# Optimization experiments

Measured on AMD Instinct MI355X. Metric: run time of the kernel, lower is better.

## Reference

```python
import jax, jax.numpy as jnp
import numpy as np

BLOCK_SIZE = 32
# NVFP4 decode table: index bit3 = sign, bits0-2 = magnitude code
DECODE = jnp.array([0.0, 0.5, 1.0, 1.5, 2.0, 3.0, 4.0, 6.0,
                    -0.0, -0.5, -1.0, -1.5, -2.0, -3.0, -4.0, -6.0], dtype=jnp.float32)

N_OUT, K_IN = 16384, 4096


def setup_inputs() -> dict:
    key = jax.random.key(0)
    k1, k2, k3, k4 = jax.random.split(key, 4)
    x = jax.random.normal(k1, (4, 512, K_IN), dtype=jnp.float32)
    # packed uint8 stored as int32 in [0, 256)
    weight_packed = jax.random.randint(k2, (N_OUT, K_IN // 2), 0, 256, dtype=jnp.int32)
    # per-block positive scales (block_max / 6.0 in the original)
    weight_scales = jax.random.uniform(k3, (N_OUT, K_IN // BLOCK_SIZE), dtype=jnp.float32,
                                       minval=1e-3, maxval=5e-2)
    bias = jax.random.normal(k4, (N_OUT,), dtype=jnp.float32) * 0.02
    return {"x": x, "weight_packed": weight_packed, "weight_scales": weight_scales, "bias": bias}


def _dequant(weight_packed, weight_scales):
    # unpack: low nibble -> even K index, high nibble -> odd K index
    low = DECODE[weight_packed & 15]           # [N, K//2]
    high = DECODE[(weight_packed >> 4) & 15]   # [N, K//2]
    n = weight_packed.shape[0]
    w = jnp.stack([low, high], axis=-1).reshape(n, -1)  # [N, K], interleaved
    # expand per-block scales along K
    scales = jnp.repeat(weight_scales, BLOCK_SIZE, axis=1)  # [N, K]
    return w * scales


def reference(x, weight_packed, weight_scales, bias):
    w = _dequant(weight_packed, weight_scales)            # [N, K]
    out = jnp.einsum('bsk,nk->bsn', x, w) + bias          # [B, S, N]
    # activation='gelu' -> F.gelu(approximate='tanh')
    return jax.nn.gelu(out, approximate=True)
```

## Files before the change

### kernel.cpp

```cpp
#include <hip/hip_runtime.h>
#include <hip/hip_bf16.h>

typedef short bf16x8 __attribute__((ext_vector_type(8)));
typedef float f32x4 __attribute__((ext_vector_type(4)));

#define K_DIM 4096
#define N_DIM 16384
#define M_DIM 2048
#define STRIPE 16384
#define TSTRIDE (64 * STRIPE)
#define WSB_BYTES ((size_t)N_DIM * K_DIM * 2)
#define WSA_BYTES ((size_t)M_DIM * K_DIM * 2)

__device__ __forceinline__ unsigned f2bf(float f) {
    unsigned u = __builtin_bit_cast(unsigned, f);
    u += 0x7FFFu + ((u >> 16) & 1u);
    return u >> 16;
}

__device__ __forceinline__ float dec4(unsigned c, float s) {
    unsigned mag = c & 7u;
    unsigned u = (mag >= 2u) ? ((((mag >> 1) + 126u) << 23) | ((mag & 1u) << 22))
                             : (mag == 1u ? 0x3F000000u : 0u);
    u |= (c & 8u) << 28;
    return __builtin_bit_cast(float, u) * s;
}

__device__ __forceinline__ float fexp2(float x) {
    float r; asm("v_exp_f32 %0, %1" : "=v"(r) : "v"(x)); return r;
}
__device__ __forceinline__ float gelu_tanh(float v) {
    float c = v + 0.044715f * v * v * v;
    float x = fminf(-2.3022084f * c, 80.0f);
    float t = fexp2(x);
    float th = (1.0f - t) * __builtin_amdgcn_rcpf(1.0f + t);
    return 0.5f * v * (1.0f + th);
}

__global__ __launch_bounds__(256) void dequant_w(const int* __restrict__ wp,
                                                 const float* __restrict__ wsc,
                                                 unsigned char* __restrict__ dst) {
    int t = blockIdx.x * 256 + threadIdx.x;
    int n = t >> 9;
    int ck = t & 511;
    int kstep = ck >> 3, s = ck & 7;
    int nt = n >> 7, r = n & 127;

    const int4 p4 = *reinterpret_cast<const int4*>(wp + (size_t)n * (K_DIM / 2) + kstep * 32 + s * 4);
    float scale = wsc[(size_t)n * (K_DIM / 32) + kstep * 2 + (s >> 2)];

    const int pv[4] = {p4.x, p4.y, p4.z, p4.w};
    unsigned o[8];
    #pragma unroll
    for (int j = 0; j < 4; ++j) {
        unsigned b = (unsigned)pv[j] & 255u;
        o[2 * j]     = f2bf(dec4(b & 15u, scale));
        o[2 * j + 1] = f2bf(dec4((b >> 4) & 15u, scale));
    }
    uint4 v;
    v.x = o[0] | (o[1] << 16);
    v.y = o[2] | (o[3] << 16);
    v.z = o[4] | (o[5] << 16);
    v.w = o[6] | (o[7] << 16);

    size_t off = (size_t)(nt * 64 + kstep) * STRIPE
               + (size_t)r * 128 + (size_t)((s ^ (r & 7)) << 4);
    *reinterpret_cast<uint4*>(dst + off) = v;
}

__global__ __launch_bounds__(256) void conv_x(const float* __restrict__ x,
                                              unsigned char* __restrict__ dst) {
    int t = blockIdx.x * 256 + threadIdx.x;
    int m = t >> 9;
    int ck = t & 511;
    int kstep = ck >> 3, s = ck & 7;
    int mt = m >> 7, r = m & 127;

    const float4* xp = reinterpret_cast<const float4*>(x + (size_t)m * K_DIM + kstep * 64 + s * 8);
    float4 a = xp[0], b = xp[1];
    uint4 v;
    v.x = f2bf(a.x) | (f2bf(a.y) << 16);
    v.y = f2bf(a.z) | (f2bf(a.w) << 16);
    v.z = f2bf(b.x) | (f2bf(b.y) << 16);
    v.w = f2bf(b.z) | (f2bf(b.w) << 16);

    size_t off = (size_t)(mt * 64 + kstep) * STRIPE
               + (size_t)r * 128 + (size_t)((s ^ (r & 7)) << 4);
    *reinterpret_cast<uint4*>(dst + off) = v;
}


__global__ __launch_bounds__(512, 2) void gemm_bf16_256(
    const unsigned char* __restrict__ wsA,
    const unsigned char* __restrict__ wsB,
    const float* __restrict__ bias,
    float* __restrict__ out)
{
    __shared__ unsigned char lds[131072];

    int id = blockIdx.x;
    int wg = (id & 7) * 64 + (id >> 3);
    int MT = wg & 7;
    int NT = wg >> 3;

    const int tid  = threadIdx.x;
    const int lane = tid & 63;
    const int w    = tid >> 6;
    const int wm   = w >> 2;
    const int wn   = w & 3;
    const int fr   = lane & 15;
    const int fg   = lane >> 4;

    const unsigned char* gA = wsA + (size_t)(2 * MT) * TSTRIDE;
    const unsigned char* gB = wsB + (size_t)(2 * NT) * TSTRIDE;

    int addrA[8];
    #pragma unroll
    for (int mi = 0; mi < 8; ++mi) {
        int row = wm * 128 + mi * 16 + fr;
        int L = row >> 1;
        addrA[mi] = L * 128 + (((((row & 1) << 2) | fg) ^ (L & 7)) << 4);
    }
    int addrB[4];
    #pragma unroll
    for (int ni = 0; ni < 4; ++ni) {
        int row = wn * 64 + ni * 16 + fr;
        int L = row >> 1;
        addrB[ni] = L * 128 + (((((row & 1) << 2) | fg) ^ (L & 7)) << 4);
    }

    int offST[2][2];
    #pragma unroll
    for (int j = 0; j < 2; ++j) {
        int c = w * 2 + j;
        int L = c * 8 + (lane >> 3);
        int p = lane & 7;
        int sl = p ^ (L & 7);
        int h = sl >> 2, fgs = sl & 3;
        int row = 2 * L + h;
        #pragma unroll
        for (int kb = 0; kb < 2; ++kb)
            offST[j][kb] = (row >> 7) * TSTRIDE + (row & 127) * 128
                         + ((((kb << 2) | fgs) ^ (row & 7)) << 4);
    }

#define GLDS(SRC, DOFF) __builtin_amdgcn_global_load_lds(                          \
        (const __attribute__((address_space(1))) unsigned int*)(SRC),              \
        (__attribute__((address_space(3))) unsigned int*)(&lds[DOFF]), 16, 0, 0)

#define STAGE_A(KSOFF, KB, SLOT) do {                                              \
        GLDS(gA + (KSOFF) + offST[0][KB], ((SLOT) << 14) + (w * 2 + 0) * 1024);    \
        GLDS(gA + (KSOFF) + offST[1][KB], ((SLOT) << 14) + (w * 2 + 1) * 1024);    \
    } while (0)
#define STAGE_B(KSOFF, KB, SLOT) do {                                              \
        GLDS(gB + (KSOFF) + offST[0][KB], 65536 + ((SLOT) << 14) + (w * 2 + 0) * 1024); \
        GLDS(gB + (KSOFF) + offST[1][KB], 65536 + ((SLOT) << 14) + (w * 2 + 1) * 1024); \
    } while (0)

#define READ_PF(PA, PB, SLOT) do {                                                 \
        const unsigned char* La_ = lds + ((SLOT) << 14);                           \
        const unsigned char* Lb_ = lds + 65536 + ((SLOT) << 14);                   \
        _Pragma("unroll") for (int ni = 0; ni < 4; ++ni)                           \
            PB[ni] = *reinterpret_cast<const bf16x8*>(Lb_ + addrB[ni]);            \
        _Pragma("unroll") for (int mi = 0; mi < 4; ++mi)                           \
            PA[mi] = *reinterpret_cast<const bf16x8*>(La_ + addrA[mi]);            \
    } while (0)

#define READ_KA(SLOT) do {                                                         \
        const unsigned char* Lk_ = lds + ((SLOT) << 14);                           \
        _Pragma("unroll") for (int mi = 0; mi < 4; ++mi)                           \
            ka[mi] = *reinterpret_cast<const bf16x8*>(Lk_ + addrA[4 + mi]);        \
    } while (0)

    f32x4 acc[8][4];
    #pragma unroll
    for (int mi = 0; mi < 8; ++mi)
        #pragma unroll
        for (int ni = 0; ni < 4; ++ni)
            acc[mi][ni] = (f32x4){0.f, 0.f, 0.f, 0.f};

    bf16x8 pa0[4], pb0[4], pa1[4], pb1[4];
    bf16x8 ka[4];

    STAGE_A(0, 0, 0);        STAGE_B(0, 0, 0);
    STAGE_A(0, 1, 1);        STAGE_B(0, 1, 1);
    STAGE_A(STRIPE, 0, 2);   STAGE_B(STRIPE, 0, 2);
    asm volatile("s_waitcnt vmcnt(4)" ::: "memory");
    __builtin_amdgcn_sched_barrier(0);
    __builtin_amdgcn_s_barrier();
    __builtin_amdgcn_sched_barrier(0);
    READ_PF(pa0, pb0, 0);
    READ_KA(0);

#define TILE_BODY(RSLOT, NSLOT, PA, PB, NPA, NPB, DO_STG, STKS, STKB, SSLOT, DO_PF, VMN) do { \
        if (DO_STG) STAGE_A(STKS, STKB, SSLOT);                                    \
        __builtin_amdgcn_s_setprio(1);                                             \
        _Pragma("unroll") for (int mi = 0; mi < 4; ++mi)                           \
            _Pragma("unroll") for (int ni = 0; ni < 4; ++ni)                       \
                acc[mi][ni] = __builtin_amdgcn_mfma_f32_16x16x32_bf16(             \
                    PA[mi], PB[ni], acc[mi][ni], 0, 0, 0);                         \
        __builtin_amdgcn_s_setprio(0);                                             \
        if (DO_STG) STAGE_B(STKS, STKB, SSLOT);                                    \
        if (DO_PF) READ_PF(NPA, NPB, NSLOT);                                       \
        __builtin_amdgcn_s_setprio(1);                                             \
        _Pragma("unroll") for (int mi = 0; mi < 4; ++mi)                           \
            _Pragma("unroll") for (int ni = 0; ni < 4; ++ni)                       \
                acc[4 + mi][ni] = __builtin_amdgcn_mfma_f32_16x16x32_bf16(         \
                    ka[mi], PB[ni], acc[4 + mi][ni], 0, 0, 0);                     \
        __builtin_amdgcn_s_setprio(0);                                             \
        if (DO_PF) READ_KA(NSLOT);                                                 \
        if ((VMN) >= 0) {                                                          \
            if ((VMN) == 4)      asm volatile("s_waitcnt vmcnt(4)" ::: "memory");  \
            else                 asm volatile("s_waitcnt vmcnt(0)" ::: "memory");  \
            __builtin_amdgcn_sched_barrier(0);                                     \
            __builtin_amdgcn_s_barrier();                                          \
            __builtin_amdgcn_sched_barrier(0);                                     \
        }                                                                          \
    } while (0)

    for (int tp = 0; tp < 62; ++tp) {
        const int scur = (tp & 1) << 1;
        const int ks1 = (tp + 1) * STRIPE;
        const int ks2 = (tp + 2) * STRIPE;
        TILE_BODY(scur,     scur ^ 1, pa0, pb0, pa1, pb1, 1, ks1, 1, scur ^ 3, 1, 4);
        TILE_BODY(scur ^ 1, scur ^ 2, pa1, pb1, pa0, pb0, 1, ks2, 0, scur,     1, 4);
    }
    TILE_BODY(0, 1, pa0, pb0, pa1, pb1, 1, 63 * STRIPE, 1, 3, 1, 4);
    TILE_BODY(1, 2, pa1, pb1, pa0, pb0, 0, 0, 0, 0, 1, 0);
    TILE_BODY(2, 3, pa0, pb0, pa1, pb1, 0, 0, 0, 0, 1, 0);
    TILE_BODY(3, 0, pa1, pb1, pa0, pb0, 0, 0, 0, 0, 0, -1);

    const int bm0 = MT * 256, bn0 = NT * 256;
    #pragma unroll
    for (int mi = 0; mi < 8; ++mi) {
        int row = bm0 + wm * 128 + mi * 16 + fg * 4;
        #pragma unroll
        for (int ni = 0; ni < 4; ++ni) {
            int col = bn0 + wn * 64 + ni * 16 + fr;
            float bv = bias[col];
            float* op = out + (size_t)row * N_DIM + col;
            #pragma unroll
            for (int q = 0; q < 4; ++q) {
                float v = acc[mi][ni][q] + bv;
                op[(size_t)q * N_DIM] = gelu_tanh(v);
            }
        }
    }
#undef TILE_BODY
#undef READ_KA
#undef READ_PF
#undef STAGE_A
#undef STAGE_B
#undef GLDS
}

__global__ __launch_bounds__(256, 2) void nvfp4_gemm(
    const float* __restrict__ x,
    const int*   __restrict__ wp,
    const float* __restrict__ wscale,
    const float* __restrict__ bias,
    float* __restrict__ out)
{
    __shared__ uint4  lsA[128 * 8];
    __shared__ uint4  lsB[128 * 8];
    __shared__ float2 lut[256];

    const int tid = threadIdx.x;
    {
        static const float dectab[16] = {0.f, 0.5f, 1.f, 1.5f, 2.f, 3.f, 4.f, 6.f,
                                         -0.f,-0.5f,-1.f,-1.5f,-2.f,-3.f,-4.f,-6.f};
        lut[tid] = make_float2(dectab[tid & 15], dectab[(tid >> 4) & 15]);
    }

    const int bn0 = blockIdx.x * 128;
    const int bm0 = blockIdx.y * 128;
    const int r = tid >> 1;
    const int h = tid & 1;

    const float4* xp = reinterpret_cast<const float4*>(x + (size_t)(bm0 + r) * K_DIM) + h * 8;
    const uint4*  bp = reinterpret_cast<const uint4*>(wp + (size_t)(bn0 + r) * (K_DIM / 2)) + h * 4;
    const float*  sp = wscale + (size_t)(bn0 + r) * (K_DIM / 32) + h;

    float4 ax[8];
    uint4  bx[4];
    float  scale;
    #pragma unroll
    for (int j = 0; j < 8; ++j) ax[j] = xp[j];
    #pragma unroll
    for (int q = 0; q < 4; ++q) bx[q] = bp[q];
    scale = sp[0];

    f32x4 acc[4][4];
    #pragma unroll
    for (int mi = 0; mi < 4; ++mi)
        #pragma unroll
        for (int ni = 0; ni < 4; ++ni)
            acc[mi][ni] = (f32x4){0.f, 0.f, 0.f, 0.f};

    const int lane = tid & 63;
    const int wid  = tid >> 6;
    const int wm0  = (wid >> 1) * 64;
    const int wn0  = (wid & 1) * 64;
    const int fr   = lane & 15;
    const int fg   = lane >> 4;

    __syncthreads();

    for (int kt = 0; kt < 64; ++kt) {
        #pragma unroll
        for (int j = 0; j < 4; ++j) {
            float4 f0 = ax[2 * j], f1 = ax[2 * j + 1];
            uint4 v;
            v.x = f2bf(f0.x) | (f2bf(f0.y) << 16);
            v.y = f2bf(f0.z) | (f2bf(f0.w) << 16);
            v.z = f2bf(f1.x) | (f2bf(f1.y) << 16);
            v.w = f2bf(f1.z) | (f2bf(f1.w) << 16);
            lsA[(r * 8 + h * 4 + j) ^ (r & 7)] = v;
        }
        #pragma unroll
        for (int q = 0; q < 4; ++q) {
            uint4 p = bx[q];
            float2 d0 = lut[p.x & 255];
            float2 d1 = lut[p.y & 255];
            float2 d2 = lut[p.z & 255];
            float2 d3 = lut[p.w & 255];
            uint4 v;
            v.x = f2bf(d0.x * scale) | (f2bf(d0.y * scale) << 16);
            v.y = f2bf(d1.x * scale) | (f2bf(d1.y * scale) << 16);
            v.z = f2bf(d2.x * scale) | (f2bf(d2.y * scale) << 16);
            v.w = f2bf(d3.x * scale) | (f2bf(d3.y * scale) << 16);
            lsB[(r * 8 + h * 4 + q) ^ (r & 7)] = v;
        }
        __syncthreads();

        if (kt + 1 < 64) {
            #pragma unroll
            for (int j = 0; j < 8; ++j) ax[j] = xp[(kt + 1) * 16 + j];
            #pragma unroll
            for (int q = 0; q < 4; ++q) bx[q] = bp[(kt + 1) * 8 + q];
            scale = sp[(kt + 1) * 2];
        }

        #pragma unroll
        for (int kk = 0; kk < 2; ++kk) {
            bf16x8 af[4], bfr[4];
            #pragma unroll
            for (int mi = 0; mi < 4; ++mi) {
                int row = wm0 + mi * 16 + fr;
                af[mi] = __builtin_bit_cast(bf16x8, lsA[(row * 8 + kk * 4 + fg) ^ (row & 7)]);
            }
            #pragma unroll
            for (int ni = 0; ni < 4; ++ni) {
                int row = wn0 + ni * 16 + fr;
                bfr[ni] = __builtin_bit_cast(bf16x8, lsB[(row * 8 + kk * 4 + fg) ^ (row & 7)]);
            }
            #pragma unroll
            for (int mi = 0; mi < 4; ++mi)
                #pragma unroll
                for (int ni = 0; ni < 4; ++ni)
                    acc[mi][ni] = __builtin_amdgcn_mfma_f32_16x16x32_bf16(
                        af[mi], bfr[ni], acc[mi][ni], 0, 0, 0);
        }
        __syncthreads();
    }

    #pragma unroll
    for (int mi = 0; mi < 4; ++mi) {
        int row = bm0 + wm0 + mi * 16 + fg * 4;
        #pragma unroll
        for (int ni = 0; ni < 4; ++ni) {
            int col = bn0 + wn0 + ni * 16 + fr;
            float bv = bias[col];
            float* op = out + (size_t)row * N_DIM + col;
            #pragma unroll
            for (int q = 0; q < 4; ++q) {
                float v = acc[mi][ni][q] + bv;
                op[(size_t)q * N_DIM] = gelu_tanh(v);
            }
        }
    }
}

extern "C" void kernel_launch(void* const* d_in, const int* in_sizes, int n_in,
                              void* d_out, int out_size, void* d_ws, size_t ws_size,
                              hipStream_t stream) {
    const float* x    = (const float*)d_in[0];
    const int*   wp   = (const int*)d_in[1];
    const float* wsc  = (const float*)d_in[2];
    const float* bias = (const float*)d_in[3];
    float*       out  = (float*)d_out;
    (void)in_sizes; (void)n_in; (void)out_size;

    if (ws_size >= WSB_BYTES + WSA_BYTES) {
        unsigned char* wsB = (unsigned char*)d_ws;
        unsigned char* wsA = wsB + WSB_BYTES;
        dequant_w<<<(N_DIM * (K_DIM / 8)) / 256, 256, 0, stream>>>(wp, wsc, wsB);
        conv_x<<<(M_DIM * (K_DIM / 8)) / 256, 256, 0, stream>>>(x, wsA);
        gemm_bf16_256<<<(M_DIM / 256) * (N_DIM / 256), 512, 0, stream>>>(wsA, wsB, bias, out);
    } else {
        dim3 grid(N_DIM / 128, M_DIM / 128);
        nvfp4_gemm<<<grid, 256, 0, stream>>>(x, wp, wsc, bias, out);
    }
}
```

Baseline: 296.8 us.

## Fuse dequant and activation conversion into GEMM with ticketed producer workgroups

Merges the weight dequant and x-to-bf16 conversion kernels into the GEMM launch. The first workgroup to claim each 256-row A or B panel via atomicCAS converts it into the workspace, publishes a done flag, and every workgroup spin-waits on the flags for its two panels before running the GEMM. The aim is to remove two kernel launches and overlap conversion with compute. The cost is a memset of the flags, spin-wait stalls, and a deadlock risk if producers are not resident. The intermediate-size workspace branch now falls back to the slow kernel, which looks unintended.

```diff
diff --git a/kernel.cpp b/kernel.cpp
--- a/kernel.cpp
+++ b/kernel.cpp
@@ -11,6 +11,7 @@
 #define TSTRIDE (64 * STRIPE)
 #define WSB_BYTES ((size_t)N_DIM * K_DIM * 2)
 #define WSA_BYTES ((size_t)M_DIM * K_DIM * 2)
+#define NUNITS 72
 
 __device__ __forceinline__ unsigned f2bf(float f) {
     unsigned u = __builtin_bit_cast(unsigned, f);
@@ -90,13 +91,18 @@
 }
 
 
-__global__ __launch_bounds__(512, 2) void gemm_bf16_256(
-    const unsigned char* __restrict__ wsA,
-    const unsigned char* __restrict__ wsB,
+__global__ __launch_bounds__(512, 2) void gemm_fused(
+    const int*   __restrict__ wp,
+    const float* __restrict__ wsc,
+    const float* __restrict__ x,
+    unsigned char* wsA,
+    unsigned char* wsB,
+    int* flags,
     const float* __restrict__ bias,
     float* __restrict__ out)
 {
     __shared__ unsigned char lds[131072];
+    __shared__ int s_role[2];
 
     int id = blockIdx.x;
     int wg = (id & 7) * 64 + (id >> 3);
@@ -110,6 +116,78 @@
     const int wn   = w & 3;
     const int fr   = lane & 15;
     const int fg   = lane >> 4;
+
+    int* tickets = flags;
+    int* done    = flags + NUNITS;
+    const int uA = MT;
+    const int uB = 8 + NT;
+
+    if (tid == 0) {
+        s_role[0] = (atomicCAS(&tickets[uA], 0, 1) == 0);
+        s_role[1] = (atomicCAS(&tickets[uB], 0, 1) == 0);
+    }
+    __syncthreads();
+
+    if (s_role[0]) {
+        for (int it = 0; it < 256; ++it) {
+            int g = it * 512 + tid;
+            int m = MT * 256 + (g >> 9);
+            int ck = g & 511;
+            int kstep = ck >> 3, s = ck & 7;
+            int mt = m >> 7, r = m & 127;
+            const float4* xp = reinterpret_cast<const float4*>(x + (size_t)m * K_DIM + kstep * 64 + s * 8);
+            float4 a = xp[0], b = xp[1];
+            uint4 v;
+            v.x = f2bf(a.x) | (f2bf(a.y) << 16);
+            v.y = f2bf(a.z) | (f2bf(a.w) << 16);
+            v.z = f2bf(b.x) | (f2bf(b.y) << 16);
+            v.w = f2bf(b.z) | (f2bf(b.w) << 16);
+            size_t off = (size_t)(mt * 64 + kstep) * STRIPE
+                       + (size_t)r * 128 + (size_t)((s ^ (r & 7)) << 4);
+            *reinterpret_cast<uint4*>(wsA + off) = v;
+        }
+    }
+    if (s_role[1]) {
+        for (int it = 0; it < 256; ++it) {
+            int g = it * 512 + tid;
+            int n = NT * 256 + (g >> 9);
+            int ck = g & 511;
+            int kstep = ck >> 3, s = ck & 7;
+            int nt = n >> 7, r = n & 127;
+            const int4 p4 = *reinterpret_cast<const int4*>(wp + (size_t)n * (K_DIM / 2) + kstep * 32 + s * 4);
+            float scale = wsc[(size_t)n * (K_DIM / 32) + kstep * 2 + (s >> 2)];
+            const int pv[4] = {p4.x, p4.y, p4.z, p4.w};
+            unsigned o[8];
+            #pragma unroll
+            for (int j = 0; j < 4; ++j) {
+                unsigned b = (unsigned)pv[j] & 255u;
+                o[2 * j]     = f2bf(dec4(b & 15u, scale));
+                o[2 * j + 1] = f2bf(dec4((b >> 4) & 15u, scale));
+            }
+            uint4 v;
+            v.x = o[0] | (o[1] << 16);
+            v.y = o[2] | (o[3] << 16);
+            v.z = o[4] | (o[5] << 16);
+            v.w = o[6] | (o[7] << 16);
+            size_t off = (size_t)(nt * 64 + kstep) * STRIPE
+                       + (size_t)r * 128 + (size_t)((s ^ (r & 7)) << 4);
+            *reinterpret_cast<uint4*>(wsB + off) = v;
+        }
+    }
+    if (s_role[0] || s_role[1]) {
+        __syncthreads();
+        if (tid == 0) {
+            __threadfence();
+            if (s_role[0]) atomicExch(&done[uA], 1);
+            if (s_role[1]) atomicExch(&done[uB], 1);
+        }
+    }
+    if (tid == 0) {
+        while (atomicAdd(&done[uA], 0) == 0) __builtin_amdgcn_s_sleep(8);
+        while (atomicAdd(&done[uB], 0) == 0) __builtin_amdgcn_s_sleep(8);
+    }
+    __syncthreads();
+    __threadfence();
 
     const unsigned char* gA = wsA + (size_t)(2 * MT) * TSTRIDE;
     const unsigned char* gB = wsB + (size_t)(2 * NT) * TSTRIDE;
@@ -391,12 +469,20 @@
     float*       out  = (float*)d_out;
     (void)in_sizes; (void)n_in; (void)out_size;
 
-    if (ws_size >= WSB_BYTES + WSA_BYTES) {
+    if (ws_size >= WSB_BYTES + WSA_BYTES + 1024) {
+        unsigned char* wsB = (unsigned char*)d_ws;
+        unsigned char* wsA = wsB + WSB_BYTES;
+        int* flags = (int*)(wsA + WSA_BYTES);
+        hipMemsetAsync(flags, 0, 1024, stream);
+        gemm_fused<<<(M_DIM / 256) * (N_DIM / 256), 512, 0, stream>>>(
+            wp, wsc, x, wsA, wsB, flags, bias, out);
+    } else if (ws_size >= WSB_BYTES + WSA_BYTES) {
         unsigned char* wsB = (unsigned char*)d_ws;
         unsigned char* wsA = wsB + WSB_BYTES;
         dequant_w<<<(N_DIM * (K_DIM / 8)) / 256, 256, 0, stream>>>(wp, wsc, wsB);
         conv_x<<<(M_DIM * (K_DIM / 8)) / 256, 256, 0, stream>>>(x, wsA);
-        gemm_bf16_256<<<(M_DIM / 256) * (N_DIM / 256), 512, 0, stream>>>(wsA, wsB, bias, out);
+        dim3 grid(N_DIM / 128, M_DIM / 128);
+        nvfp4_gemm<<<grid, 256, 0, stream>>>(x, wp, wsc, bias, out);
     } else {
         dim3 grid(N_DIM / 128, M_DIM / 128);
         nvfp4_gemm<<<grid, 256, 0, stream>>>(x, wp, wsc, bias, out);
```

Result: slower. 930.8 us (+213.6%).
